# Optimization experiments

Hardware: AMD Instinct MI355X
Metric: run time of the kernel (lower is better)

The kernel has to match this reference:

```python
import jax, jax.numpy as jnp
import numpy as np

B_GRAPHS = 16      # number of graphs in batch
NPG = 8192         # nodes per graph
N = B_GRAPHS * NPG # 131072 total nodes
F_DIM = 64         # node feature dim
K_CLUST = 16       # n_clusters
DEG = 32           # avg degree
E = N * DEG        # 4,194,304 edges


def setup_inputs() -> dict:
    key = jax.random.key(0)
    k1, k2, k3, k4, k5 = jax.random.split(key, 5)
    x = jax.random.normal(k1, (N, F_DIM), jnp.float32)
    W = jax.random.normal(k2, (F_DIM, K_CLUST), jnp.float32) / np.sqrt(F_DIM)
    b = jnp.zeros((K_CLUST,), jnp.float32)
    # edges constrained within each graph -> block-diagonal adjacency (PyG batching)
    g = jnp.repeat(jnp.arange(B_GRAPHS, dtype=jnp.int32), E // B_GRAPHS)
    edge_row = g * NPG + jax.random.randint(k3, (E,), 0, NPG, jnp.int32)
    edge_col = g * NPG + jax.random.randint(k4, (E,), 0, NPG, jnp.int32)
    edge_weight = jax.random.uniform(k5, (E,), jnp.float32)
    return {"x": x, "W": W, "b": b, "edge_weight": edge_weight,
            "edge_row": edge_row, "edge_col": edge_col, "num_graphs": B_GRAPHS}


def _forward(x, W, b, edge_weight, edge_row, edge_col, num_graphs):
    Ntot, Fd = x.shape
    K = W.shape[1]
    Bn = num_graphs
    n = Ntot // Bn  # equal-size graphs (ptr = n * arange(B+1))

    s = x @ W + b                                   # [N,K] cluster logits
    xb = x.reshape(Bn, n, Fd)
    sb = s.reshape(Bn, n, K)
    # out_x = selu(s^T @ x_bd), block b = s_b^T x_b, then hsplit_and_vstack -> [B*K, F]
    out_x = jax.nn.selu(jnp.einsum('bnk,bnf->bkf', sb, xb)).reshape(Bn * K, Fd)

    ss = jax.nn.softmax(s, axis=-1)                 # softmaxed assignments
    ssb = ss.reshape(Bn, n, K)

    # degree d = adj.sum(axis=0)  (column sums over COO edges)
    d = jax.ops.segment_sum(edge_weight, edge_col, num_segments=Ntot)   # [N]
    m2 = d.reshape(Bn, n).sum(1)                    # total degree per graph [B]

    # A @ C via edge scatter: (A C)[row] += w * C[col]
    AC = jax.ops.segment_sum(edge_weight[:, None] * ss[edge_col], edge_row,
                             num_segments=Ntot)     # [N,K]
    # out_adj blocks: C_b^T A_b C_b  -> [B,K,K]
    out_adj = jnp.einsum('bnk,bnl->bkl', ssb, AC.reshape(Bn, n, K))

    # dS_b = C_b^T d_b  (Ca/Cb blocks); normalizer gets m_inv twice in torch code
    dS = jnp.einsum('bn,bnk->bk', d.reshape(Bn, n), ssb)                # [B,K]
    spectral_loss = -jnp.mean(jnp.einsum('bkk->b', out_adj) / m2
                              - (dS ** 2).sum(1) / (m2 ** 2))

    sqrt_K = jnp.sqrt(jnp.float32(K))
    cluster_size = ssb.sum(1)                        # [B,K]
    cluster_loss = jnp.mean(jnp.sqrt((cluster_size ** 2).sum(1)) / n * sqrt_K - 1.0)

    # CC blocks: C_b^T C_b; ortho = mean_b || CC_b/||CC_b||_F - I/sqrt(K) ||_F
    CC = jnp.einsum('bnk,bnl->bkl', ssb, ssb)        # [B,K,K]
    CC_norm = jnp.sqrt((CC ** 2).sum((1, 2)))        # Frobenius norm per block
    eye_div_k = jnp.eye(K, dtype=x.dtype) / sqrt_K
    ortho_loss = jnp.mean(jnp.sqrt(
        ((CC / CC_norm[:, None, None] - eye_div_k) ** 2).sum((1, 2))))

    # mask diagonal and degree-normalize pooled adjacency
    oa = out_adj * (1.0 - jnp.eye(K, dtype=x.dtype))
    dd = jnp.sqrt(oa.sum(2)) + 1e-12                 # row sums per block [B,K]
    out_adj_norm = oa / (dd[:, :, None] * dd[:, None, :])

    return out_x, out_adj_norm, spectral_loss, cluster_loss, ortho_loss


def reference(x, W, b, edge_weight, edge_row, edge_col, num_graphs):
    return _forward(x, W, b, edge_weight, edge_row, edge_col, num_graphs)
```

## Files before the change

### kernel.cpp

```cpp
#include <hip/hip_runtime.h>
#include <math.h>

#define F_DIM 64
#define K_CL 16
#define B_GR 16
#define SROW 72

typedef _Float16 h16;
using f16x8 = __attribute__((ext_vector_type(8))) _Float16;
using f32x4 = __attribute__((ext_vector_type(4))) float;

__global__ __launch_bounds__(256) void k_fused(
    const float* __restrict__ x, const float* __restrict__ W, const float* __restrict__ bvec,
    h16* __restrict__ ssh, float* __restrict__ outx, float* __restrict__ CCb)
{
    __shared__ float Wl[F_DIM * K_CL];
    __shared__ float bl[K_CL];
    __shared__ __align__(16) h16 stage[4][(16 + 16 + 64) * SROW];

    int t = threadIdx.x;
    for (int idx = t; idx < F_DIM * K_CL; idx += 256) Wl[idx] = W[idx];
    if (t < K_CL) bl[t] = bvec[t];
    __syncthreads();

    int wid = t >> 6, lane = t & 63;
    h16* Sg = stage[wid];
    h16* Cg = Sg + 16 * SROW;
    h16* Xg = Cg + 16 * SROW;

    size_t i = (size_t)blockIdx.x * 256 + t;
    float s[16];
#pragma unroll
    for (int k = 0; k < 16; ++k) s[k] = bl[k];

    const float4* xp = reinterpret_cast<const float4*>(x + i * F_DIM);
#pragma unroll
    for (int j = 0; j < 16; ++j) {
        float4 q = xp[j];
        float xf[4] = {q.x, q.y, q.z, q.w};
#pragma unroll
        for (int ff = 0; ff < 4; ++ff) {
            int f = j * 4 + ff;
            float xv = xf[ff];
            Xg[f * SROW + lane] = (h16)xv;
            const float4* wr = reinterpret_cast<const float4*>(&Wl[f * K_CL]);
            float4 w0 = wr[0], w1 = wr[1], w2 = wr[2], w3 = wr[3];
            s[0]  += xv * w0.x; s[1]  += xv * w0.y; s[2]  += xv * w0.z; s[3]  += xv * w0.w;
            s[4]  += xv * w1.x; s[5]  += xv * w1.y; s[6]  += xv * w1.z; s[7]  += xv * w1.w;
            s[8]  += xv * w2.x; s[9]  += xv * w2.y; s[10] += xv * w2.z; s[11] += xv * w2.w;
            s[12] += xv * w3.x; s[13] += xv * w3.y; s[14] += xv * w3.z; s[15] += xv * w3.w;
        }
    }

#pragma unroll
    for (int k = 0; k < 16; ++k) Sg[k * SROW + lane] = (h16)s[k];

    float m = s[0];
#pragma unroll
    for (int k = 1; k < 16; ++k) m = fmaxf(m, s[k]);
    float sum = 0.f;
#pragma unroll
    for (int k = 0; k < 16; ++k) { s[k] = __expf(s[k] - m); sum += s[k]; }
    float inv = 1.0f / sum;
#pragma unroll
    for (int k = 0; k < 16; ++k) s[k] *= inv;

    f16x8 h0, h1;
#pragma unroll
    for (int k = 0; k < 8; ++k) { h0[k] = (h16)s[k]; h1[k] = (h16)s[k + 8]; }
#pragma unroll
    for (int k = 0; k < 8; ++k) {
        Cg[k * SROW + lane] = h0[k];
        Cg[(k + 8) * SROW + lane] = h1[k];
    }
    f16x8* hp = reinterpret_cast<f16x8*>(ssh + i * K_CL);
    hp[0] = h0;
    hp[1] = h1;

    int q4 = lane >> 4, mm = lane & 15;
    f32x4 accO[4] = {{0.f,0.f,0.f,0.f},{0.f,0.f,0.f,0.f},{0.f,0.f,0.f,0.f},{0.f,0.f,0.f,0.f}};
    f32x4 accC = {0.f, 0.f, 0.f, 0.f};
#pragma unroll
    for (int h = 0; h < 2; ++h) {
        f16x8 aO = *(const f16x8*)&Sg[mm * SROW + h * 32 + q4 * 8];
        f16x8 aC = *(const f16x8*)&Cg[mm * SROW + h * 32 + q4 * 8];
        accC = __builtin_amdgcn_mfma_f32_16x16x32_f16(aC, aC, accC, 0, 0, 0);
#pragma unroll
        for (int ft = 0; ft < 4; ++ft) {
            f16x8 bO = *(const f16x8*)&Xg[(ft * 16 + mm) * SROW + h * 32 + q4 * 8];
            accO[ft] = __builtin_amdgcn_mfma_f32_16x16x32_f16(aO, bO, accO[ft], 0, 0, 0);
        }
    }
    __syncthreads();

    float* redO = (float*)&stage[0][0];
    float* redC = redO + 4096;
#pragma unroll
    for (int ft = 0; ft < 4; ++ft)
#pragma unroll
        for (int rg = 0; rg < 4; ++rg)
            redO[wid * 1024 + (q4 * 4 + rg) * 64 + ft * 16 + mm] = accO[ft][rg];
#pragma unroll
    for (int rg = 0; rg < 4; ++rg)
        redC[wid * 256 + (q4 * 4 + rg) * 16 + mm] = accC[rg];
    __syncthreads();

    int g = blockIdx.x >> 5;
#pragma unroll
    for (int it = 0; it < 4; ++it) {
        int idx = t + it * 256;
        float v = redO[idx] + redO[1024 + idx] + redO[2048 + idx] + redO[3072 + idx];
        atomicAdd(outx + g * 1024 + idx, v);
    }
    {
        float v = redC[t] + redC[256 + t] + redC[512 + t] + redC[768 + t];
        atomicAdd(CCb + g * 256 + t, v);
    }
}

__global__ __launch_bounds__(256) void k_edge(
    const int* __restrict__ erow, const int* __restrict__ ecol, const float* __restrict__ ew,
    const h16* __restrict__ ssh, float* __restrict__ oadj,
    int edges_per_block, int edges_per_graph, int nmask)
{
    __shared__ float CCl[256];
    __shared__ __align__(16) h16 stageE[4][32 * SROW];
    int t = threadIdx.x;
    CCl[t] = 0.f;
    __syncthreads();

    int bid = blockIdx.x;
    int xcd = bid & 7;
    int slot = bid >> 3;
    int graph = xcd + 8 * (slot & 1);
    int chunk = slot >> 1;

    int wid = t >> 6, lane = t & 63;
    int q4 = lane >> 4, mm = lane & 15;
    h16* Ag = stageE[wid];
    h16* Bg = Ag + 16 * SROW;

    int epw = edges_per_block >> 2;
    size_t base = (size_t)graph * edges_per_graph
                + (size_t)chunk * edges_per_block
                + (size_t)wid * epw;

    const f16x8* sshp = reinterpret_cast<const f16x8*>(ssh);
    f32x4 acc = {0.f, 0.f, 0.f, 0.f};

    for (int e0 = 0; e0 < epw; e0 += 64) {
        size_t eb = base + e0 + lane;
        int   r = erow[eb] & nmask;
        int   c = ecol[eb] & nmask;
        float w = ew[eb];

        f16x8 a0 = sshp[2 * (size_t)r];
        f16x8 a1 = sshp[2 * (size_t)r + 1];
        f16x8 b0 = sshp[2 * (size_t)c];
        f16x8 b1 = sshp[2 * (size_t)c + 1];
        h16 wh = (h16)w;
#pragma unroll
        for (int k = 0; k < 8; ++k) { a0[k] *= wh; a1[k] *= wh; }

#pragma unroll
        for (int k = 0; k < 8; ++k) {
            Ag[k * SROW + lane]       = a0[k];
            Ag[(k + 8) * SROW + lane] = a1[k];
            Bg[k * SROW + lane]       = b0[k];
            Bg[(k + 8) * SROW + lane] = b1[k];
        }

#pragma unroll
        for (int h = 0; h < 2; ++h) {
            f16x8 af = *(const f16x8*)&Ag[mm * SROW + h * 32 + q4 * 8];
            f16x8 bf = *(const f16x8*)&Bg[mm * SROW + h * 32 + q4 * 8];
            acc = __builtin_amdgcn_mfma_f32_16x16x32_f16(af, bf, acc, 0, 0, 0);
        }
    }

#pragma unroll
    for (int rg = 0; rg < 4; ++rg)
        atomicAdd(&CCl[(q4 * 4 + rg) * 16 + mm], acc[rg]);
    __syncthreads();
    atomicAdd(oadj + graph * 256 + t, CCl[t]);
}

__global__ __launch_bounds__(256) void k_final(
    const float* __restrict__ outx, const float* __restrict__ oadj,
    const float* __restrict__ CCb, float* __restrict__ out, int npg)
{
    int t = threadIdx.x;
    int gid = blockIdx.x * 256 + t;
    {
        float v = outx[gid];
        float r = (v > 0.f) ? (1.0507009873554805f * v)
                            : (1.0507009873554805f * 1.6732632423543772f * (__expf(v) - 1.0f));
        out[gid] = r;
    }

    if (blockIdx.x != 0) return;

    int b = t >> 4, k = t & 15;
    const float* oar = oadj + b * 256 + k * 16;
    const float* ccr = CCb + b * 256 + k * 16;

    float rowsum_off = 0.f, trace_c = 0.f, rowsum_all = 0.f, fro2 = 0.f, colsum = 0.f;
    float csv = 0.f;
#pragma unroll
    for (int l = 0; l < 16; ++l) {
        float v = oar[l];
        rowsum_all += v;
        if (l == k) trace_c = v; else rowsum_off += v;
        float c = ccr[l];
        fro2 += c * c;
        csv += c;
        colsum += oadj[b * 256 + l * 16 + k];
    }
    float dd = sqrtf(rowsum_off) + 1e-12f;
    __shared__ float ddl[B_GR * K_CL];
    ddl[t] = dd;

    float ds2 = colsum * colsum, cs2 = csv * csv;
    float tr = trace_c, m2 = rowsum_all;
#pragma unroll
    for (int msk = 8; msk >= 1; msk >>= 1) {
        tr   += __shfl_xor(tr,   msk, 16);
        ds2  += __shfl_xor(ds2,  msk, 16);
        cs2  += __shfl_xor(cs2,  msk, 16);
        fro2 += __shfl_xor(fro2, msk, 16);
        m2   += __shfl_xor(m2,   msk, 16);
    }
    float invfro = 1.0f / sqrtf(fro2);
    float osum = 0.f;
#pragma unroll
    for (int l = 0; l < 16; ++l) {
        float v = ccr[l] * invfro - ((l == k) ? 0.25f : 0.f);
        osum += v * v;
    }
#pragma unroll
    for (int msk = 8; msk >= 1; msk >>= 1) osum += __shfl_xor(osum, msk, 16);

    __shared__ float sp_s[B_GR], cl_s[B_GR], or_s[B_GR];
    if (k == 0) {
        sp_s[b] = tr / m2 - ds2 / (m2 * m2);
        cl_s[b] = sqrtf(cs2) / (float)npg * 4.0f - 1.0f;
        or_s[b] = sqrtf(osum);
    }
    __syncthreads();
    if (t == 0) {
        float a = 0.f, c = 0.f, o = 0.f;
        for (int i = 0; i < B_GR; ++i) { a += sp_s[i]; c += cl_s[i]; o += or_s[i]; }
        out[20480] = -a / 16.f;
        out[20481] = c / 16.f;
        out[20482] = o / 16.f;
    }

#pragma unroll
    for (int l = 0; l < 16; ++l) {
        float v = (l == k) ? 0.f : oar[l] / (dd * ddl[b * 16 + l]);
        out[16384 + b * 256 + k * 16 + l] = v;
    }
}

extern "C" void kernel_launch(void* const* d_in, const int* in_sizes, int n_in,
                              void* d_out, int out_size, void* d_ws, size_t ws_size,
                              hipStream_t stream)
{
    const float* x    = (const float*)d_in[0];
    const float* W    = (const float*)d_in[1];
    const float* bvec = (const float*)d_in[2];
    const float* ew   = (const float*)d_in[3];
    const int* erow   = (const int*)d_in[4];
    const int* ecol   = (const int*)d_in[5];

    int Ntot = in_sizes[0] / F_DIM;
    size_t E = (size_t)in_sizes[3];
    int npg  = Ntot / B_GR;
    int edges_per_graph = (int)(E / B_GR);
    int nmask = Ntot - 1;

    const int ADJ_BLOCKS = 2048;
    int edges_per_block = (int)(E / ADJ_BLOCKS);

    char* ws = (char*)d_ws;
    size_t o = 0;
    h16*   ssh   = (h16*)(ws + o);   o += (size_t)Ntot * 16 * 2;
    size_t zoff = o;
    float* outx  = (float*)(ws + o); o += (size_t)B_GR * 1024 * 4;
    float* oadj  = (float*)(ws + o); o += (size_t)B_GR * 256 * 4;
    float* CCb   = (float*)(ws + o); o += (size_t)B_GR * 256 * 4;

    hipMemsetAsync(ws + zoff, 0, o - zoff, stream);

    k_fused<<<Ntot / 256, 256, 0, stream>>>(x, W, bvec, ssh, outx, CCb);
    k_edge<<<ADJ_BLOCKS, 256, 0, stream>>>(erow, ecol, ew, ssh, oadj,
                                           edges_per_block, edges_per_graph, nmask);
    k_final<<<64, 256, 0, stream>>>(outx, oadj, CCb, (float*)d_out, npg);
}
```

Measured before the change: 169.9 us.

## Store softmax assignments as 8-bit fp16-high bytes and use FP32 FMA for pooling

The softmax assignment table is now stored as one byte per cluster (the rounded top byte of the fp16 value, an e5m2-like format), halving the table the edge kernel gathers at random. The edge kernel unpacks these bytes, interleaves A and B operands in one LDS tile, and feeds MFMA. The node kernel drops the MFMA path for s^T x and C^T C and computes them with FP32 FMAs over shared-memory copies of the logits and softmax, re-reading x from global. Reducing assignments to 8-bit precision may raise error in out_adj and the spectral loss.

```diff
diff --git a/kernel.cpp b/kernel.cpp
--- a/kernel.cpp
+++ b/kernel.cpp
@@ -1,130 +1,155 @@
 #include <hip/hip_runtime.h>
 #include <math.h>
+#include <stdint.h>
 
 #define F_DIM 64
 #define K_CL 16
 #define B_GR 16
-#define SROW 72
+#define SR32 68
 
 typedef _Float16 h16;
 using f16x8 = __attribute__((ext_vector_type(8))) _Float16;
+using f16x2 = __attribute__((ext_vector_type(2))) _Float16;
 using f32x4 = __attribute__((ext_vector_type(4))) float;
+
+union HU { h16 f; unsigned short u; };
+union PU { uint32_t u; f16x2 v; };
+union H8 { f16x8 v; uint32_t u[4]; };
 
 __global__ __launch_bounds__(256) void k_fused(
     const float* __restrict__ x, const float* __restrict__ W, const float* __restrict__ bvec,
-    h16* __restrict__ ssh, float* __restrict__ outx, float* __restrict__ CCb)
+    uint32_t* __restrict__ ssq, float* __restrict__ outx, float* __restrict__ CCb)
 {
     __shared__ float Wl[F_DIM * K_CL];
     __shared__ float bl[K_CL];
-    __shared__ __align__(16) h16 stage[4][(16 + 16 + 64) * SROW];
+    __shared__ __align__(16) float Ss[256 * 20];
+    __shared__ __align__(16) float Cs[256 * 20];
+    __shared__ float CCl[256];
 
     int t = threadIdx.x;
     for (int idx = t; idx < F_DIM * K_CL; idx += 256) Wl[idx] = W[idx];
     if (t < K_CL) bl[t] = bvec[t];
+    CCl[t] = 0.f;
     __syncthreads();
 
     int wid = t >> 6, lane = t & 63;
-    h16* Sg = stage[wid];
-    h16* Cg = Sg + 16 * SROW;
-    h16* Xg = Cg + 16 * SROW;
-
-    size_t i = (size_t)blockIdx.x * 256 + t;
-    float s[16];
-#pragma unroll
-    for (int k = 0; k < 16; ++k) s[k] = bl[k];
-
-    const float4* xp = reinterpret_cast<const float4*>(x + i * F_DIM);
-#pragma unroll
-    for (int j = 0; j < 16; ++j) {
-        float4 q = xp[j];
-        float xf[4] = {q.x, q.y, q.z, q.w};
-#pragma unroll
-        for (int ff = 0; ff < 4; ++ff) {
-            int f = j * 4 + ff;
-            float xv = xf[ff];
-            Xg[f * SROW + lane] = (h16)xv;
-            const float4* wr = reinterpret_cast<const float4*>(&Wl[f * K_CL]);
-            float4 w0 = wr[0], w1 = wr[1], w2 = wr[2], w3 = wr[3];
-            s[0]  += xv * w0.x; s[1]  += xv * w0.y; s[2]  += xv * w0.z; s[3]  += xv * w0.w;
-            s[4]  += xv * w1.x; s[5]  += xv * w1.y; s[6]  += xv * w1.z; s[7]  += xv * w1.w;
-            s[8]  += xv * w2.x; s[9]  += xv * w2.y; s[10] += xv * w2.z; s[11] += xv * w2.w;
-            s[12] += xv * w3.x; s[13] += xv * w3.y; s[14] += xv * w3.z; s[15] += xv * w3.w;
-        }
-    }
-
-#pragma unroll
-    for (int k = 0; k < 16; ++k) Sg[k * SROW + lane] = (h16)s[k];
-
-    float m = s[0];
-#pragma unroll
-    for (int k = 1; k < 16; ++k) m = fmaxf(m, s[k]);
-    float sum = 0.f;
-#pragma unroll
-    for (int k = 0; k < 16; ++k) { s[k] = __expf(s[k] - m); sum += s[k]; }
-    float inv = 1.0f / sum;
-#pragma unroll
-    for (int k = 0; k < 16; ++k) s[k] *= inv;
-
-    f16x8 h0, h1;
-#pragma unroll
-    for (int k = 0; k < 8; ++k) { h0[k] = (h16)s[k]; h1[k] = (h16)s[k + 8]; }
-#pragma unroll
-    for (int k = 0; k < 8; ++k) {
-        Cg[k * SROW + lane] = h0[k];
-        Cg[(k + 8) * SROW + lane] = h1[k];
-    }
-    f16x8* hp = reinterpret_cast<f16x8*>(ssh + i * K_CL);
-    hp[0] = h0;
-    hp[1] = h1;
-
-    int q4 = lane >> 4, mm = lane & 15;
-    f32x4 accO[4] = {{0.f,0.f,0.f,0.f},{0.f,0.f,0.f,0.f},{0.f,0.f,0.f,0.f},{0.f,0.f,0.f,0.f}};
-    f32x4 accC = {0.f, 0.f, 0.f, 0.f};
-#pragma unroll
-    for (int h = 0; h < 2; ++h) {
-        f16x8 aO = *(const f16x8*)&Sg[mm * SROW + h * 32 + q4 * 8];
-        f16x8 aC = *(const f16x8*)&Cg[mm * SROW + h * 32 + q4 * 8];
-        accC = __builtin_amdgcn_mfma_f32_16x16x32_f16(aC, aC, accC, 0, 0, 0);
-#pragma unroll
-        for (int ft = 0; ft < 4; ++ft) {
-            f16x8 bO = *(const f16x8*)&Xg[(ft * 16 + mm) * SROW + h * 32 + q4 * 8];
-            accO[ft] = __builtin_amdgcn_mfma_f32_16x16x32_f16(aO, bO, accO[ft], 0, 0, 0);
-        }
-    }
-    __syncthreads();
-
-    float* redO = (float*)&stage[0][0];
-    float* redC = redO + 4096;
-#pragma unroll
-    for (int ft = 0; ft < 4; ++ft)
-#pragma unroll
-        for (int rg = 0; rg < 4; ++rg)
-            redO[wid * 1024 + (q4 * 4 + rg) * 64 + ft * 16 + mm] = accO[ft][rg];
-#pragma unroll
-    for (int rg = 0; rg < 4; ++rg)
-        redC[wid * 256 + (q4 * 4 + rg) * 16 + mm] = accC[rg];
-    __syncthreads();
-
-    int g = blockIdx.x >> 5;
+    int bid = blockIdx.x;
+
+    {
+        size_t i = (size_t)bid * 256 + t;
+        float s[16];
+#pragma unroll
+        for (int k = 0; k < 16; ++k) s[k] = bl[k];
+
+        const float4* xp = reinterpret_cast<const float4*>(x + i * F_DIM);
+#pragma unroll
+        for (int j = 0; j < 16; ++j) {
+            float4 q = xp[j];
+            float xf[4] = {q.x, q.y, q.z, q.w};
+#pragma unroll
+            for (int ff = 0; ff < 4; ++ff) {
+                int f = j * 4 + ff;
+                float xv = xf[ff];
+                const float4* wr = reinterpret_cast<const float4*>(&Wl[f * K_CL]);
+                float4 w0 = wr[0], w1 = wr[1], w2 = wr[2], w3 = wr[3];
+                s[0]  += xv * w0.x; s[1]  += xv * w0.y; s[2]  += xv * w0.z; s[3]  += xv * w0.w;
+                s[4]  += xv * w1.x; s[5]  += xv * w1.y; s[6]  += xv * w1.z; s[7]  += xv * w1.w;
+                s[8]  += xv * w2.x; s[9]  += xv * w2.y; s[10] += xv * w2.z; s[11] += xv * w2.w;
+                s[12] += xv * w3.x; s[13] += xv * w3.y; s[14] += xv * w3.z; s[15] += xv * w3.w;
+            }
+        }
+
+        float4* sp = reinterpret_cast<float4*>(&Ss[t * 20]);
+        sp[0] = make_float4(s[0], s[1], s[2], s[3]);
+        sp[1] = make_float4(s[4], s[5], s[6], s[7]);
+        sp[2] = make_float4(s[8], s[9], s[10], s[11]);
+        sp[3] = make_float4(s[12], s[13], s[14], s[15]);
+
+        float m = s[0];
+#pragma unroll
+        for (int k = 1; k < 16; ++k) m = fmaxf(m, s[k]);
+        float sum = 0.f;
+#pragma unroll
+        for (int k = 0; k < 16; ++k) { s[k] = __expf(s[k] - m); sum += s[k]; }
+        float inv = 1.0f / sum;
+#pragma unroll
+        for (int k = 0; k < 16; ++k) s[k] *= inv;
+
+        float4* cp = reinterpret_cast<float4*>(&Cs[t * 20]);
+        cp[0] = make_float4(s[0], s[1], s[2], s[3]);
+        cp[1] = make_float4(s[4], s[5], s[6], s[7]);
+        cp[2] = make_float4(s[8], s[9], s[10], s[11]);
+        cp[3] = make_float4(s[12], s[13], s[14], s[15]);
+
+        uint32_t g[4];
+#pragma unroll
+        for (int i4 = 0; i4 < 4; ++i4) {
+            uint32_t acc = 0;
+#pragma unroll
+            for (int j4 = 0; j4 < 4; ++j4) {
+                HU h; h.f = (h16)s[i4 * 4 + j4];
+                uint32_t u = h.u;
+                uint32_t b = (u + 0x7Fu + ((u >> 7) & 1u)) >> 8;
+                acc |= (b & 0xFFu) << (8 * j4);
+            }
+            g[i4] = acc;
+        }
+        *reinterpret_cast<uint4*>(ssq + i * 4) = make_uint4(g[0], g[1], g[2], g[3]);
+    }
+
+    float accx[16];
+#pragma unroll
+    for (int k = 0; k < 16; ++k) accx[k] = 0.f;
+    float accc[4] = {0.f, 0.f, 0.f, 0.f};
+    int g4 = lane >> 4, l = lane & 15;
+    size_t xbase = ((size_t)bid * 256 + wid * 64) * F_DIM;
+
+    for (int j = 0; j < 64; ++j) {
+        int node = wid * 64 + j;
+        float xv = x[xbase + (size_t)j * F_DIM + lane];
+        const float4* sp = reinterpret_cast<const float4*>(&Ss[node * 20]);
+        float4 s0 = sp[0], s1 = sp[1], s2 = sp[2], s3 = sp[3];
+        accx[0]  += s0.x * xv; accx[1]  += s0.y * xv; accx[2]  += s0.z * xv; accx[3]  += s0.w * xv;
+        accx[4]  += s1.x * xv; accx[5]  += s1.y * xv; accx[6]  += s1.z * xv; accx[7]  += s1.w * xv;
+        accx[8]  += s2.x * xv; accx[9]  += s2.y * xv; accx[10] += s2.z * xv; accx[11] += s2.w * xv;
+        accx[12] += s3.x * xv; accx[13] += s3.y * xv; accx[14] += s3.z * xv; accx[15] += s3.w * xv;
+
+        float ssl = Cs[node * 20 + l];
+        float4 sq = *reinterpret_cast<const float4*>(&Cs[node * 20 + g4 * 4]);
+        accc[0] += sq.x * ssl;
+        accc[1] += sq.y * ssl;
+        accc[2] += sq.z * ssl;
+        accc[3] += sq.w * ssl;
+    }
+
+#pragma unroll
+    for (int j4 = 0; j4 < 4; ++j4)
+        atomicAdd(&CCl[(g4 * 4 + j4) * 16 + l], accc[j4]);
+    __syncthreads();
+
+    float* redx = Ss;
+#pragma unroll
+    for (int k = 0; k < 16; ++k) redx[wid * 1024 + k * 64 + lane] = accx[k];
+    __syncthreads();
+
+    int g = bid >> 5;
+    float* dst = outx + g * (K_CL * F_DIM);
 #pragma unroll
     for (int it = 0; it < 4; ++it) {
         int idx = t + it * 256;
-        float v = redO[idx] + redO[1024 + idx] + redO[2048 + idx] + redO[3072 + idx];
-        atomicAdd(outx + g * 1024 + idx, v);
-    }
-    {
-        float v = redC[t] + redC[256 + t] + redC[512 + t] + redC[768 + t];
-        atomicAdd(CCb + g * 256 + t, v);
-    }
+        float v = redx[idx] + redx[1024 + idx] + redx[2048 + idx] + redx[3072 + idx];
+        atomicAdd(dst + idx, v);
+    }
+    atomicAdd(&CCb[g * 256 + t], CCl[t]);
 }
 
 __global__ __launch_bounds__(256) void k_edge(
     const int* __restrict__ erow, const int* __restrict__ ecol, const float* __restrict__ ew,
-    const h16* __restrict__ ssh, float* __restrict__ oadj,
+    const uint32_t* __restrict__ ssq, float* __restrict__ oadj,
     int edges_per_block, int edges_per_graph, int nmask)
 {
     __shared__ float CCl[256];
-    __shared__ __align__(16) h16 stageE[4][32 * SROW];
+    __shared__ __align__(16) uint32_t AB[4][16 * SR32];
     int t = threadIdx.x;
     CCl[t] = 0.f;
     __syncthreads();
@@ -137,15 +162,13 @@
 
     int wid = t >> 6, lane = t & 63;
     int q4 = lane >> 4, mm = lane & 15;
-    h16* Ag = stageE[wid];
-    h16* Bg = Ag + 16 * SROW;
+    uint32_t* ABw = AB[wid];
 
     int epw = edges_per_block >> 2;
     size_t base = (size_t)graph * edges_per_graph
                 + (size_t)chunk * edges_per_block
                 + (size_t)wid * epw;
 
-    const f16x8* sshp = reinterpret_cast<const f16x8*>(ssh);
     f32x4 acc = {0.f, 0.f, 0.f, 0.f};
 
     for (int e0 = 0; e0 < epw; e0 += 64) {
@@ -154,27 +177,54 @@
         int   c = ecol[eb] & nmask;
         float w = ew[eb];
 
-        f16x8 a0 = sshp[2 * (size_t)r];
-        f16x8 a1 = sshp[2 * (size_t)r + 1];
-        f16x8 b0 = sshp[2 * (size_t)c];
-        f16x8 b1 = sshp[2 * (size_t)c + 1];
-        h16 wh = (h16)w;
-#pragma unroll
-        for (int k = 0; k < 8; ++k) { a0[k] *= wh; a1[k] *= wh; }
-
-#pragma unroll
-        for (int k = 0; k < 8; ++k) {
-            Ag[k * SROW + lane]       = a0[k];
-            Ag[(k + 8) * SROW + lane] = a1[k];
-            Bg[k * SROW + lane]       = b0[k];
-            Bg[(k + 8) * SROW + lane] = b1[k];
+        uint4 ga = *reinterpret_cast<const uint4*>(ssq + (size_t)r * 4);
+        uint4 gb = *reinterpret_cast<const uint4*>(ssq + (size_t)c * 4);
+
+        uint32_t pa[8], pb[8];
+        uint32_t gaw[4] = {ga.x, ga.y, ga.z, ga.w};
+        uint32_t gbw[4] = {gb.x, gb.y, gb.z, gb.w};
+#pragma unroll
+        for (int i4 = 0; i4 < 4; ++i4) {
+            pa[2 * i4]     = (gaw[i4] << 8) & 0xFF00FF00u;
+            pa[2 * i4 + 1] =  gaw[i4]       & 0xFF00FF00u;
+            pb[2 * i4]     = (gbw[i4] << 8) & 0xFF00FF00u;
+            pb[2 * i4 + 1] =  gbw[i4]       & 0xFF00FF00u;
+        }
+
+        HU wh; wh.f = (h16)w;
+        PU wp; wp.u = (uint32_t)wh.u | ((uint32_t)wh.u << 16);
+#pragma unroll
+        for (int i8 = 0; i8 < 8; ++i8) {
+            PU a; a.u = pa[i8];
+            a.v = a.v * wp.v;
+            pa[i8] = a.u;
+        }
+
+#pragma unroll
+        for (int i4 = 0; i4 < 4; ++i4) {
+            uint32_t alo = pa[2 * i4], ahi = pa[2 * i4 + 1];
+            uint32_t blo = pb[2 * i4], bhi = pb[2 * i4 + 1];
+            ABw[(4 * i4 + 0) * SR32 + lane] = (alo & 0xFFFFu) | (blo << 16);
+            ABw[(4 * i4 + 1) * SR32 + lane] = (ahi & 0xFFFFu) | (bhi << 16);
+            ABw[(4 * i4 + 2) * SR32 + lane] = (alo >> 16) | (bhi & 0u) | (blo & 0xFFFF0000u);
+            ABw[(4 * i4 + 3) * SR32 + lane] = (ahi >> 16) | (bhi & 0xFFFF0000u);
         }
 
 #pragma unroll
         for (int h = 0; h < 2; ++h) {
-            f16x8 af = *(const f16x8*)&Ag[mm * SROW + h * 32 + q4 * 8];
-            f16x8 bf = *(const f16x8*)&Bg[mm * SROW + h * 32 + q4 * 8];
-            acc = __builtin_amdgcn_mfma_f32_16x16x32_f16(af, bf, acc, 0, 0, 0);
+            const uint32_t* rowp = &ABw[mm * SR32 + h * 32 + q4 * 8];
+            uint4 p0 = *reinterpret_cast<const uint4*>(rowp);
+            uint4 p1 = *reinterpret_cast<const uint4*>(rowp + 4);
+            H8 Af, Bf;
+            Af.u[0] = (p0.x & 0xFFFFu) | (p0.y << 16);
+            Bf.u[0] = (p0.x >> 16)     | (p0.y & 0xFFFF0000u);
+            Af.u[1] = (p0.z & 0xFFFFu) | (p0.w << 16);
+            Bf.u[1] = (p0.z >> 16)     | (p0.w & 0xFFFF0000u);
+            Af.u[2] = (p1.x & 0xFFFFu) | (p1.y << 16);
+            Bf.u[2] = (p1.x >> 16)     | (p1.y & 0xFFFF0000u);
+            Af.u[3] = (p1.z & 0xFFFFu) | (p1.w << 16);
+            Bf.u[3] = (p1.z >> 16)     | (p1.w & 0xFFFF0000u);
+            acc = __builtin_amdgcn_mfma_f32_16x16x32_f16(Af.v, Bf.v, acc, 0, 0, 0);
         }
     }
 
@@ -284,16 +334,16 @@
 
     char* ws = (char*)d_ws;
     size_t o = 0;
-    h16*   ssh   = (h16*)(ws + o);   o += (size_t)Ntot * 16 * 2;
+    uint32_t* ssq = (uint32_t*)(ws + o); o += (size_t)Ntot * 16;
     size_t zoff = o;
-    float* outx  = (float*)(ws + o); o += (size_t)B_GR * 1024 * 4;
-    float* oadj  = (float*)(ws + o); o += (size_t)B_GR * 256 * 4;
-    float* CCb   = (float*)(ws + o); o += (size_t)B_GR * 256 * 4;
+    float* outx = (float*)(ws + o); o += (size_t)B_GR * 1024 * 4;
+    float* oadj = (float*)(ws + o); o += (size_t)B_GR * 256 * 4;
+    float* CCb  = (float*)(ws + o); o += (size_t)B_GR * 256 * 4;
 
     hipMemsetAsync(ws + zoff, 0, o - zoff, stream);
 
-    k_fused<<<Ntot / 256, 256, 0, stream>>>(x, W, bvec, ssh, outx, CCb);
-    k_edge<<<ADJ_BLOCKS, 256, 0, stream>>>(erow, ecol, ew, ssh, oadj,
+    k_fused<<<Ntot / 256, 256, 0, stream>>>(x, W, bvec, ssq, outx, CCb);
+    k_edge<<<ADJ_BLOCKS, 256, 0, stream>>>(erow, ecol, ew, ssq, oadj,
                                            edges_per_block, edges_per_graph, nmask);
     k_final<<<64, 256, 0, stream>>>(outx, oadj, CCb, (float*)d_out, npg);
 }
```

After: 176.4 us. +3.8%, slower.
